# Optimization experiments

Measured on AMD Instinct MI355X. Metric: run time of the kernel, lower is better.

The kernel has to match this reference:

```python
import jax, jax.numpy as jnp
import numpy as np

COMMITMENT_COST = 0.25
EPS = 1e-10


def setup_inputs() -> dict:
    key = jax.random.key(0)
    k0, k1, k2, k3 = jax.random.split(key, 4)
    return {
        "data": jax.random.normal(k0, (16, 4096, 256), dtype=jnp.float32),
        "codebook0": jax.random.normal(k1, (512, 256), dtype=jnp.float32),
        "codebook1": jax.random.normal(k2, (512, 256), dtype=jnp.float32),
        "codebook2": jax.random.normal(k3, (512, 256), dtype=jnp.float32),
        "using": 0,
    }


def _vq_stage(x, cb, beta):
    # x: [N, D] residual; cb: [K, D] codebook
    d = (jnp.sum(x * x, axis=-1, keepdims=True)
         - 2.0 * jnp.einsum('nd,kd->nk', x, cb)
         + jnp.sum(cb * cb, axis=-1))
    idx = jnp.argmin(d, axis=-1)                       # [N]
    enc = jax.nn.one_hot(idx, cb.shape[0], dtype=x.dtype)  # [N, K]
    q = cb[idx]                                        # [N, D] gather
    e_latent = jnp.mean((jax.lax.stop_gradient(q) - x) ** 2)
    q_latent = jnp.mean((q - jax.lax.stop_gradient(x)) ** 2)
    loss = q_latent + beta * e_latent
    q_st = x + jax.lax.stop_gradient(q - x)            # straight-through
    avg_probs = jnp.mean(enc, axis=0)
    entropy = -jnp.sum(avg_probs * jnp.log(avg_probs + EPS))
    return q_st, enc, loss, entropy


def reference(data, codebook0, codebook1, codebook2, using):
    D = data.shape[-1]
    input_shape = data.shape
    flat = data.reshape(-1, D)                         # [N, D]
    codebooks = [codebook0, codebook1, codebook2]
    quantized = jnp.zeros_like(flat)
    total_loss = jnp.float32(0.0)
    total_entropy = jnp.float32(0.0)
    encodings = []
    for stage_cnt, cb in enumerate(codebooks, start=1):
        sub_q, enc, loss, entropy = _vq_stage(flat - quantized, cb, COMMITMENT_COST)
        quantized = quantized + sub_q
        encodings.append(enc)
        total_loss = total_loss + loss
        total_entropy = total_entropy + entropy
        if stage_cnt == using:
            break
    quantized = quantized.reshape(input_shape)
    return (quantized, encodings[0], encodings[1], encodings[2], total_loss, total_entropy)
```

## Files before the change

kernel.cpp:

```cpp
#include <hip/hip_runtime.h>
#include <math.h>

#define NROWS  65536
#define DDIM   256
#define KCODES 512
#define NTH    512
#define NSTAGE 3
#define MARGIN  0.5f
#define MAXFLAG 65536
#define NLOSS   256
#define MB      64
#define RB      8

typedef __attribute__((ext_vector_type(8))) short short8v;
typedef __attribute__((ext_vector_type(4))) float f32x4;

__device__ __forceinline__ unsigned short f2bf(float x) {
  unsigned int u = __float_as_uint(x);
  unsigned int r = (u + 0x7fffu + ((u >> 16) & 1u)) >> 16;
  return (unsigned short)r;
}

__device__ __forceinline__ void glds16(const void* g, void* l) {
  __builtin_amdgcn_global_load_lds(
      (const __attribute__((address_space(1))) unsigned int*)g,
      (__attribute__((address_space(3))) unsigned int*)l, 16, 0, 0);
}

__device__ __forceinline__ float np_sumsq256(const float* p) {
#pragma clang fp contract(off)
  float blk[2];
#pragma unroll
  for (int b = 0; b < 2; ++b) {
    const float* a = p + b * 128;
    float v[16];
#pragma unroll
    for (int l = 0; l < 16; ++l) {
      float p0a = a[l] * a[l];
      float p0b = a[64 + l] * a[64 + l];
      float P0 = p0a + p0b;
      float p1a = a[16 + l] * a[16 + l];
      float p1b = a[80 + l] * a[80 + l];
      float P1 = p1a + p1b;
      float p2a = a[32 + l] * a[32 + l];
      float p2b = a[96 + l] * a[96 + l];
      float P2 = p2a + p2b;
      float p3a = a[48 + l] * a[48 + l];
      float p3b = a[112 + l] * a[112 + l];
      float P3 = p3a + p3b;
      v[l] = (P0 + P1) + (P2 + P3);
    }
    float s1[8];
#pragma unroll
    for (int l = 0; l < 8; ++l) s1[l] = v[l] + v[l + 8];
    float s2[4];
#pragma unroll
    for (int l = 0; l < 4; ++l) s2[l] = s1[l] + s1[l + 4];
    float s3_0 = s2[0] + s2[2];
    float s3_1 = s2[1] + s2[3];
    blk[b] = s3_0 + s3_1;
  }
  return blk[0] + blk[1];
}

__global__ void cc_np_k(const float* __restrict__ c0, const float* __restrict__ c1,
                        const float* __restrict__ c2, float* __restrict__ cc) {
  int t = blockIdx.x * blockDim.x + threadIdx.x;
  if (t >= NSTAGE * KCODES) return;
  const float* cb = (t < KCODES) ? c0 : (t < 2 * KCODES ? c1 : c2);
  cc[t] = np_sumsq256(cb + (size_t)(t & (KCODES - 1)) * DDIM);
}

__global__ void split_cb_k(const float* __restrict__ c0, const float* __restrict__ c1,
                           const float* __restrict__ c2,
                           unsigned short* __restrict__ Ch) {
  int t = blockIdx.x * 256 + threadIdx.x;
  if (t >= NSTAGE * KCODES * 32) return;
  int s = t / (KCODES * 32);
  int rem = t - s * KCODES * 32;
  int code = rem >> 5;
  int gran = rem & 31;
  int chunk = gran >> 2;
  int g = gran & 3;
  int ctile = code >> 6;
  int ct = (code >> 4) & 3;
  int c16 = code & 15;
  const float* cb = (s == 0) ? c0 : (s == 1 ? c1 : c2);
  const float* src = cb + (size_t)code * DDIM + gran * 8;
  unsigned short hv[8];
#pragma unroll
  for (int j = 0; j < 8; ++j) hv[j] = f2bf(src[j]);
  size_t off = (size_t)s * 262144 +
               ((((size_t)(ctile * 8 + chunk) * 4 + ct) * 64) + (g * 16 + c16)) * 16;
  *(uint4*)((char*)Ch + off) = *(uint4*)hv;
}

__global__ __launch_bounds__(256) void chain_k(
    const float* __restrict__ data,
    const float* __restrict__ cbA, const float* __restrict__ cbB,
    const int* __restrict__ idxA, const int* __restrict__ idxB,
    int stage, char* __restrict__ AhG) {
  const int t = blockIdx.x * 256 + threadIdx.x;
  const int r = t >> 5;
  const int g = t & 31;
  const int k0 = g * 8;
  float res[8];
  {
#pragma clang fp contract(off)
    const size_t base = (size_t)r * DDIM + k0;
    int iA = 0, iB = 0;
    if (stage >= 1) iA = idxA[r];
    if (stage == 2) iB = idxB[r];
#pragma unroll
    for (int half = 0; half < 2; ++half) {
      float4 dv = *(const float4*)(data + base + half * 4);
      float x1[4] = {dv.x, dv.y, dv.z, dv.w};
      float rr[4];
      if (stage == 0) {
#pragma unroll
        for (int j = 0; j < 4; ++j) rr[j] = x1[j];
      } else {
        float4 av = *(const float4*)(cbA + (size_t)iA * DDIM + k0 + half * 4);
        float af[4] = {av.x, av.y, av.z, av.w};
        float a[4];
#pragma unroll
        for (int j = 0; j < 4; ++j) a[j] = x1[j] + (af[j] - x1[j]);
        if (stage == 2) {
          float4 bv = *(const float4*)(cbB + (size_t)iB * DDIM + k0 + half * 4);
          float bf[4] = {bv.x, bv.y, bv.z, bv.w};
#pragma unroll
          for (int j = 0; j < 4; ++j) {
            float x2 = x1[j] - a[j];
            float qst2 = x2 + (bf[j] - x2);
            a[j] = a[j] + qst2;
          }
        }
#pragma unroll
        for (int j = 0; j < 4; ++j) rr[j] = x1[j] - a[j];
      }
#pragma unroll
      for (int j = 0; j < 4; ++j) res[half * 4 + j] = rr[j];
    }
  }
  unsigned short hv[8];
#pragma unroll
  for (int j = 0; j < 8; ++j) hv[j] = f2bf(res[j]);
  const int blk = r >> 6, lr = r & 63;
  const size_t byte = (size_t)blk * 32768 + ((lr * 512 + g * 16) ^ ((lr & 7) << 4));
  *(uint4*)(AhG + byte) = *(uint4*)hv;
}

#define A_H_OFF 0
#define RED_OFF 32768
#define SMEM_SZ 40960

__global__ __launch_bounds__(NTH, 1) void gemm_k(
    const char* __restrict__ AhG,
    const unsigned short* __restrict__ Chf,
    const float* __restrict__ ccs,
    int* __restrict__ idx_out, unsigned int* __restrict__ flagcnt,
    int* __restrict__ flagrows) {
  __shared__ char smem[SMEM_SZ];

  const int tid = threadIdx.x;
  const int lane = tid & 63;
  const int w = tid >> 6;
  const int blk = blockIdx.x;
  const int rowbase = blk * MB;

  {
    const char* gh = AhG + (size_t)blk * 32768;
    const int off0 = w * 1024 + lane * 16;
#pragma unroll
    for (int rr2 = 0; rr2 < 4; ++rr2)
      glds16(gh + rr2 * 8192 + off0, smem + A_H_OFF + rr2 * 8192 + off0);
  }

  f32x4 acc[4][4];
#pragma unroll
  for (int rt = 0; rt < 4; ++rt)
#pragma unroll
    for (int ct = 0; ct < 4; ++ct) {
      acc[rt][ct].x = 0.f; acc[rt][ct].y = 0.f;
      acc[rt][ct].z = 0.f; acc[rt][ct].w = 0.f;
    }

  const int g = lane >> 4, c16 = lane & 15;
  const char* bhw = (const char*)Chf + lane * 16;

  __syncthreads();

#pragma clang loop unroll(disable)
  for (int chunk = 0; chunk < 8; ++chunk) {
    short8v ah[4];
#pragma unroll
    for (int rt = 0; rt < 4; ++rt) {
      const int row = rt * 16 + c16;
      const int byte = (row * 512 + (chunk * 4 + g) * 16) ^ ((row & 7) << 4);
      ah[rt] = *(short8v*)(smem + A_H_OFF + byte);
    }
#pragma unroll
    for (int ct = 0; ct < 4; ++ct) {
      short8v bh = *(const short8v*)(bhw + (size_t)((w * 8 + chunk) * 4 + ct) * 1024);
#pragma unroll
      for (int rt = 0; rt < 4; ++rt)
        acc[rt][ct] = __builtin_amdgcn_mfma_f32_16x16x32_bf16(ah[rt], bh, acc[rt][ct], 0, 0, 0);
    }
  }
  __syncthreads();

  float ccv[4];
#pragma unroll
  for (int ct = 0; ct < 4; ++ct) ccv[ct] = ccs[w * 64 + ct * 16 + c16];

  float* red = (float*)(smem + RED_OFF);
#pragma unroll
  for (int rt = 0; rt < 4; ++rt) {
#pragma unroll
    for (int reg = 0; reg < 4; ++reg) {
      const int row = rt * 16 + g * 4 + reg;
      float v1 = 3.0e38f, v2 = 3.0e38f;
      int i1 = 0x7fffffff;
#pragma unroll
      for (int ct = 0; ct < 4; ++ct) {
        const int col = w * 64 + ct * 16 + c16;
        float dd = ccv[ct] - 2.0f * acc[rt][ct][reg];
        if (dd < v1 || (dd == v1 && col < i1)) { v2 = v1; v1 = dd; i1 = col; }
        else if (dd < v2) v2 = dd;
      }
#pragma unroll
      for (int m = 1; m < 16; m <<= 1) {
        float ov1 = __shfl_xor(v1, m, 64);
        int oi1 = __shfl_xor(i1, m, 64);
        float ov2 = __shfl_xor(v2, m, 64);
        float worst = fmaxf(v1, ov1);
        v2 = fminf(fminf(v2, ov2), worst);
        if (ov1 < v1 || (ov1 == v1 && oi1 < i1)) { v1 = ov1; i1 = oi1; }
      }
      if (c16 == 0) {
        float* slot = red + (size_t)(row * 8 + w) * 4;
        slot[0] = v1;
        ((int*)slot)[1] = i1;
        slot[2] = v2;
      }
    }
  }
  __syncthreads();
  if (tid < MB) {
    float v1 = 3.0e38f, v2 = 3.0e38f;
    int i1 = 0x7fffffff;
#pragma unroll
    for (int ww = 0; ww < 8; ++ww) {
      const float* slot = red + (size_t)(tid * 8 + ww) * 4;
      float ov1 = slot[0];
      int oi1 = ((const int*)slot)[1];
      float ov2 = slot[2];
      float worst = fmaxf(v1, ov1);
      v2 = fminf(fminf(v2, ov2), worst);
      if (ov1 < v1 || (ov1 == v1 && oi1 < i1)) { v1 = ov1; i1 = oi1; }
    }
    const int r = rowbase + tid;
    idx_out[r] = i1;
    if (v2 - v1 < MARGIN) {
      unsigned pos = atomicAdd(flagcnt, 1u);
      if (pos < MAXFLAG) flagrows[pos] = r;
    }
  }
}

__global__ __launch_bounds__(256) void refine_k(
    const float* __restrict__ data, const float* __restrict__ cb,
    const float* __restrict__ cbA, const float* __restrict__ cbB,
    const int* __restrict__ idxA, const int* __restrict__ idxB,
    const float* __restrict__ ccs, int stage,
    const unsigned int* __restrict__ flagcnt, const int* __restrict__ flagrows,
    int* __restrict__ idx_out) {
  __shared__ float rows[RB][DDIM];
  __shared__ float xxs[RB];
  __shared__ float red_v[RB][256];
  __shared__ int red_i[RB][256];

  unsigned int n = *flagcnt;
  if (n > MAXFLAG) n = MAXFLAG;
  const int tid = threadIdx.x;

  for (unsigned base = (unsigned)blockIdx.x * RB; base < n;
       base += (unsigned)gridDim.x * RB) {
    const int nb = (int)min((unsigned)RB, n - base);

    for (int u = tid; u < nb * 64; u += 256) {
#pragma clang fp contract(off)
      const int i = u >> 6;
      const int c4 = (u & 63) * 4;
      const int r = flagrows[base + i];
      const size_t gbase = (size_t)r * DDIM + c4;
      float4 dv = *(const float4*)(data + gbase);
      float x1[4] = {dv.x, dv.y, dv.z, dv.w};
      float res[4];
      if (stage == 0) {
#pragma unroll
        for (int j = 0; j < 4; ++j) res[j] = x1[j];
      } else {
        const int iA = idxA[r];
        float4 av = *(const float4*)(cbA + (size_t)iA * DDIM + c4);
        float af[4] = {av.x, av.y, av.z, av.w};
        float a[4];
#pragma unroll
        for (int j = 0; j < 4; ++j) a[j] = x1[j] + (af[j] - x1[j]);
        if (stage == 2) {
          const int iB = idxB[r];
          float4 bv = *(const float4*)(cbB + (size_t)iB * DDIM + c4);
          float bf[4] = {bv.x, bv.y, bv.z, bv.w};
#pragma unroll
          for (int j = 0; j < 4; ++j) {
            float x2 = x1[j] - a[j];
            float qst2 = x2 + (bf[j] - x2);
            a[j] = a[j] + qst2;
          }
        }
#pragma unroll
        for (int j = 0; j < 4; ++j) res[j] = x1[j] - a[j];
      }
#pragma unroll
      for (int j = 0; j < 4; ++j) rows[i][c4 + j] = res[j];
    }
    __syncthreads();
    if (tid < nb) xxs[tid] = np_sumsq256(rows[tid]);
    __syncthreads();

    float bv[RB];
    int bi[RB];
#pragma unroll
    for (int i = 0; i < RB; ++i) { bv[i] = 3.0e38f; bi[i] = 0x7fffffff; }

#pragma clang loop unroll(disable)
    for (int h = 0; h < 2; ++h) {
#pragma clang fp contract(off)
      const int k = tid + h * 256;
      const float* crow = cb + (size_t)k * DDIM;
      float v[RB][4];
#pragma unroll
      for (int i = 0; i < RB; ++i)
#pragma unroll
        for (int l = 0; l < 4; ++l) v[i][l] = 0.f;

#pragma clang loop unroll(disable)
      for (int t = 0; t < 16; ++t) {
        float b[16];
#pragma unroll
        for (int j = 0; j < 16; ++j) b[j] = crow[t * 16 + j];
#pragma unroll
        for (int i = 0; i < RB; ++i) {
#pragma unroll
          for (int l = 0; l < 4; ++l) {
            float a0 = rows[i][t * 16 + l];
            float a1 = rows[i][t * 16 + 4 + l];
            float a2 = rows[i][t * 16 + 8 + l];
            float a3 = rows[i][t * 16 + 12 + l];
            float ab3 = a3 * b[12 + l] + v[i][l];
            float ab2 = a2 * b[8 + l] + ab3;
            float ab1 = a1 * b[4 + l] + ab2;
            v[i][l] = a0 * b[l] + ab1;
          }
        }
      }
      const float cck = ccs[k];
#pragma unroll
      for (int i = 0; i < RB; ++i) {
        float dot = (v[i][0] + v[i][1]) + (v[i][2] + v[i][3]);
        float t1 = xxs[i] - 2.0f * dot;
        float d = t1 + cck;
        if (d < bv[i] || (d == bv[i] && k < bi[i])) { bv[i] = d; bi[i] = k; }
      }
    }

#pragma unroll
    for (int i = 0; i < RB; ++i) { red_v[i][tid] = bv[i]; red_i[i][tid] = bi[i]; }
    __syncthreads();
    for (int gap = 128; gap > 0; gap >>= 1) {
      if (tid < gap) {
#pragma unroll
        for (int i = 0; i < RB; ++i) {
          float o = red_v[i][tid + gap];
          int oi = red_i[i][tid + gap];
          if (o < red_v[i][tid] || (o == red_v[i][tid] && oi < red_i[i][tid])) {
            red_v[i][tid] = o;
            red_i[i][tid] = oi;
          }
        }
      }
      __syncthreads();
    }
    if (tid < nb) idx_out[flagrows[base + tid]] = red_i[tid][0];
    __syncthreads();
  }
}

__global__ __launch_bounds__(256) void final_k(
    const float* __restrict__ data, const float* __restrict__ cb0,
    const float* __restrict__ cb1, const float* __restrict__ cb2,
    const int* __restrict__ idx0, const int* __restrict__ idx1,
    const int* __restrict__ idx2, float* __restrict__ quant,
    float* __restrict__ enc0, float* __restrict__ enc1,
    float* __restrict__ enc2, double* __restrict__ loss_slots,
    unsigned int* __restrict__ hist) {
  __shared__ double wsum[4];
  const int lane = threadIdx.x & 63;
  const int w = threadIdx.x >> 6;
  const int r = blockIdx.x * 4 + w;
  const int i0 = idx0[r], i1 = idx1[r], i2 = idx2[r];
  const size_t base = (size_t)r * DDIM + lane * 4;
  float4 dv = *(const float4*)(data + base);
  float4 c0v = *(const float4*)(cb0 + (size_t)i0 * DDIM + lane * 4);
  float4 c1v = *(const float4*)(cb1 + (size_t)i1 * DDIM + lane * 4);
  float4 c2v = *(const float4*)(cb2 + (size_t)i2 * DDIM + lane * 4);
  float df[4] = {dv.x, dv.y, dv.z, dv.w};
  float q0f[4] = {c0v.x, c0v.y, c0v.z, c0v.w};
  float q1f[4] = {c1v.x, c1v.y, c1v.z, c1v.w};
  float q2f[4] = {c2v.x, c2v.y, c2v.z, c2v.w};
  float qout[4];
  double lsum = 0.0;
  {
#pragma clang fp contract(off)
#pragma unroll
    for (int j = 0; j < 4; ++j) {
      float x1 = df[j];
      float d1 = q0f[j] - x1;
      float qst1 = x1 + d1;
      float a1 = qst1;
      float x2 = x1 - a1;
      float d2 = q1f[j] - x2;
      float qst2 = x2 + d2;
      float a2 = a1 + qst2;
      float x3 = x1 - a2;
      float d3 = q2f[j] - x3;
      float qst3 = x3 + d3;
      float a3 = a2 + qst3;
      qout[j] = a3;
      lsum += (double)d1 * d1 + (double)d2 * d2 + (double)d3 * d3;
    }
  }
  float4 qv = {qout[0], qout[1], qout[2], qout[3]};
  *(float4*)(quant + base) = qv;

#pragma unroll
  for (int off = 1; off < 64; off <<= 1) lsum += __shfl_xor(lsum, off, 64);
  if (lane == 0) {
    wsum[w] = lsum;
    enc0[(size_t)r * KCODES + i0] = 1.0f;
    atomicAdd(&hist[i0], 1u);
  } else if (lane == 1) {
    enc1[(size_t)r * KCODES + i1] = 1.0f;
    atomicAdd(&hist[KCODES + i1], 1u);
  } else if (lane == 2) {
    enc2[(size_t)r * KCODES + i2] = 1.0f;
    atomicAdd(&hist[2 * KCODES + i2], 1u);
  }
  __syncthreads();
  if (threadIdx.x == 0) {
    double bsum = (wsum[0] + wsum[1]) + (wsum[2] + wsum[3]);
    atomicAdd(&loss_slots[blockIdx.x & (NLOSS - 1)], bsum);
  }
}

__global__ void finalize_k(const unsigned int* __restrict__ hist,
                           const double* __restrict__ loss_slots,
                           float* __restrict__ out_scalars) {
  int lane = threadIdx.x;
  double te = 0.0;
  for (int s = 0; s < NSTAGE; ++s) {
    double e = 0.0;
    for (int j = 0; j < KCODES / 64; ++j) {
      int k = j * 64 + lane;
      float pf = (float)hist[s * KCODES + k] * (1.0f / 65536.0f);
      float sf = __fadd_rn(pf, 1e-10f);
      e += (double)pf * log((double)sf);
    }
#pragma unroll
    for (int off = 1; off < 64; off <<= 1) e += __shfl_xor(e, off, 64);
    te += -e;
  }
  double ls = loss_slots[lane] + loss_slots[64 + lane] +
              loss_slots[128 + lane] + loss_slots[192 + lane];
#pragma unroll
  for (int off = 1; off < 64; off <<= 1) ls += __shfl_xor(ls, off, 64);
  if (lane == 0) {
    double tl = 1.25 * ls * (1.0 / 16777216.0);
    out_scalars[0] = (float)tl;
    out_scalars[1] = (float)te;
  }
}

extern "C" void kernel_launch(void* const* d_in, const int* in_sizes, int n_in,
                              void* d_out, int out_size, void* d_ws, size_t ws_size,
                              hipStream_t stream) {
  const float* data = (const float*)d_in[0];
  const float* cb0 = (const float*)d_in[1];
  const float* cb1 = (const float*)d_in[2];
  const float* cb2 = (const float*)d_in[3];
  const float* cbs[3] = {cb0, cb1, cb2};
  float* out = (float*)d_out;
  float* quant = out;
  float* enc0 = out + (size_t)NROWS * DDIM;
  float* enc1 = enc0 + (size_t)NROWS * KCODES;
  float* enc2 = enc1 + (size_t)NROWS * KCODES;
  float* out_scalars = enc2 + (size_t)NROWS * KCODES;

  char* AhG = (char*)enc0;

  double* loss_slots = (double*)d_ws;
  unsigned int* hist = (unsigned int*)((char*)d_ws + 2048);
  unsigned int* flagcnt = (unsigned int*)((char*)d_ws + 8192);
  int* flagrows = (int*)((char*)d_ws + 8320);
  float* cc = (float*)((char*)d_ws + 794752);
  int* idx0 = (int*)((char*)d_ws + 800896);
  int* idx1 = idx0 + NROWS;
  int* idx2 = idx1 + NROWS;
  int* idxs[3] = {idx0, idx1, idx2};
  unsigned short* Ch = (unsigned short*)((char*)d_ws + 1587328);

  hipMemsetAsync(d_ws, 0, 8320, stream);

  cc_np_k<<<(NSTAGE * KCODES + 255) / 256, 256, 0, stream>>>(cb0, cb1, cb2, cc);
  split_cb_k<<<(NSTAGE * KCODES * 32 + 255) / 256, 256, 0, stream>>>(
      cb0, cb1, cb2, Ch);

  for (int s = 0; s < NSTAGE; ++s) {
    chain_k<<<NROWS * 32 / 256, 256, 0, stream>>>(
        data, cb0, cb1, idx0, idx1, s, AhG);
    gemm_k<<<NROWS / MB, NTH, 0, stream>>>(
        AhG,
        (const unsigned short*)((char*)Ch + (size_t)s * 262144),
        cc + s * KCODES, idxs[s], flagcnt + s, flagrows + s * MAXFLAG);
    refine_k<<<512, 256, 0, stream>>>(
        data, cbs[s], cb0, cb1, idx0, idx1, cc + s * KCODES, s,
        flagcnt + s, flagrows + s * MAXFLAG, idxs[s]);
  }

  hipMemsetAsync(enc0, 0, (size_t)3 * NROWS * KCODES * sizeof(float), stream);

  final_k<<<NROWS / 4, 256, 0, stream>>>(
      data, cb0, cb1, cb2, idx0, idx1, idx2, quant, enc0, enc1, enc2,
      loss_slots, hist);

  finalize_k<<<1, 64, 0, stream>>>(hist, loss_slots, out_scalars);
}
```

Before: 537.3 us.

## Use split-bf16 three-product GEMM and tighten refine margin

Splits the residuals and codebooks into high and low bf16 parts and accumulates hi*hi + hi*lo + lo*hi with MFMA, so the distance GEMM is close to fp32 accuracy. The near-tie margin that flags rows for exact fp32 refinement drops from 0.5 to 0.025, which should sharply cut the number of rows refine_k has to recompute. The cost is triple the MFMA work, twice the LDS and A-tile traffic, and an extra low-part codebook buffer in the workspace.

```diff
diff --git a/kernel.cpp b/kernel.cpp
--- a/kernel.cpp
+++ b/kernel.cpp
@@ -6,7 +6,7 @@
 #define KCODES 512
 #define NTH    512
 #define NSTAGE 3
-#define MARGIN  0.5f
+#define MARGIN  2.5e-2f
 #define MAXFLAG 65536
 #define NLOSS   256
 #define MB      64
@@ -19,6 +19,9 @@
   unsigned int u = __float_as_uint(x);
   unsigned int r = (u + 0x7fffu + ((u >> 16) & 1u)) >> 16;
   return (unsigned short)r;
+}
+__device__ __forceinline__ float bf2f(unsigned short h) {
+  return __uint_as_float(((unsigned int)h) << 16);
 }
 
 __device__ __forceinline__ void glds16(const void* g, void* l) {
@@ -73,7 +76,8 @@
 
 __global__ void split_cb_k(const float* __restrict__ c0, const float* __restrict__ c1,
                            const float* __restrict__ c2,
-                           unsigned short* __restrict__ Ch) {
+                           unsigned short* __restrict__ Ch,
+                           unsigned short* __restrict__ Cl) {
   int t = blockIdx.x * 256 + threadIdx.x;
   if (t >= NSTAGE * KCODES * 32) return;
   int s = t / (KCODES * 32);
@@ -87,19 +91,25 @@
   int c16 = code & 15;
   const float* cb = (s == 0) ? c0 : (s == 1 ? c1 : c2);
   const float* src = cb + (size_t)code * DDIM + gran * 8;
-  unsigned short hv[8];
-#pragma unroll
-  for (int j = 0; j < 8; ++j) hv[j] = f2bf(src[j]);
+  unsigned short hv[8], lv[8];
+#pragma unroll
+  for (int j = 0; j < 8; ++j) {
+    float x = src[j];
+    unsigned short h = f2bf(x);
+    hv[j] = h;
+    lv[j] = f2bf(x - bf2f(h));
+  }
   size_t off = (size_t)s * 262144 +
                ((((size_t)(ctile * 8 + chunk) * 4 + ct) * 64) + (g * 16 + c16)) * 16;
   *(uint4*)((char*)Ch + off) = *(uint4*)hv;
+  *(uint4*)((char*)Cl + off) = *(uint4*)lv;
 }
 
 __global__ __launch_bounds__(256) void chain_k(
     const float* __restrict__ data,
     const float* __restrict__ cbA, const float* __restrict__ cbB,
     const int* __restrict__ idxA, const int* __restrict__ idxB,
-    int stage, char* __restrict__ AhG) {
+    int stage, char* __restrict__ AhG, char* __restrict__ AlG) {
   const int t = blockIdx.x * 256 + threadIdx.x;
   const int r = t >> 5;
   const int g = t & 31;
@@ -142,21 +152,27 @@
       for (int j = 0; j < 4; ++j) res[half * 4 + j] = rr[j];
     }
   }
-  unsigned short hv[8];
-#pragma unroll
-  for (int j = 0; j < 8; ++j) hv[j] = f2bf(res[j]);
+  unsigned short hv[8], lv[8];
+#pragma unroll
+  for (int j = 0; j < 8; ++j) {
+    unsigned short h = f2bf(res[j]);
+    hv[j] = h;
+    lv[j] = f2bf(res[j] - bf2f(h));
+  }
   const int blk = r >> 6, lr = r & 63;
   const size_t byte = (size_t)blk * 32768 + ((lr * 512 + g * 16) ^ ((lr & 7) << 4));
   *(uint4*)(AhG + byte) = *(uint4*)hv;
+  *(uint4*)(AlG + byte) = *(uint4*)lv;
 }
 
 #define A_H_OFF 0
-#define RED_OFF 32768
-#define SMEM_SZ 40960
+#define A_L_OFF 32768
+#define RED_OFF 65536
+#define SMEM_SZ 73728
 
 __global__ __launch_bounds__(NTH, 1) void gemm_k(
-    const char* __restrict__ AhG,
-    const unsigned short* __restrict__ Chf,
+    const char* __restrict__ AhG, const char* __restrict__ AlG,
+    const unsigned short* __restrict__ Chf, const unsigned short* __restrict__ Clf,
     const float* __restrict__ ccs,
     int* __restrict__ idx_out, unsigned int* __restrict__ flagcnt,
     int* __restrict__ flagrows) {
@@ -170,10 +186,13 @@
 
   {
     const char* gh = AhG + (size_t)blk * 32768;
+    const char* gl = AlG + (size_t)blk * 32768;
     const int off0 = w * 1024 + lane * 16;
 #pragma unroll
-    for (int rr2 = 0; rr2 < 4; ++rr2)
+    for (int rr2 = 0; rr2 < 4; ++rr2) {
       glds16(gh + rr2 * 8192 + off0, smem + A_H_OFF + rr2 * 8192 + off0);
+      glds16(gl + rr2 * 8192 + off0, smem + A_L_OFF + rr2 * 8192 + off0);
+    }
   }
 
   f32x4 acc[4][4];
@@ -187,24 +206,30 @@
 
   const int g = lane >> 4, c16 = lane & 15;
   const char* bhw = (const char*)Chf + lane * 16;
+  const char* blw = (const char*)Clf + lane * 16;
 
   __syncthreads();
 
 #pragma clang loop unroll(disable)
   for (int chunk = 0; chunk < 8; ++chunk) {
-    short8v ah[4];
+    short8v ah[4], al[4];
 #pragma unroll
     for (int rt = 0; rt < 4; ++rt) {
       const int row = rt * 16 + c16;
       const int byte = (row * 512 + (chunk * 4 + g) * 16) ^ ((row & 7) << 4);
       ah[rt] = *(short8v*)(smem + A_H_OFF + byte);
+      al[rt] = *(short8v*)(smem + A_L_OFF + byte);
     }
 #pragma unroll
     for (int ct = 0; ct < 4; ++ct) {
       short8v bh = *(const short8v*)(bhw + (size_t)((w * 8 + chunk) * 4 + ct) * 1024);
-#pragma unroll
-      for (int rt = 0; rt < 4; ++rt)
+      short8v bl = *(const short8v*)(blw + (size_t)((w * 8 + chunk) * 4 + ct) * 1024);
+#pragma unroll
+      for (int rt = 0; rt < 4; ++rt) {
         acc[rt][ct] = __builtin_amdgcn_mfma_f32_16x16x32_bf16(ah[rt], bh, acc[rt][ct], 0, 0, 0);
+        acc[rt][ct] = __builtin_amdgcn_mfma_f32_16x16x32_bf16(ah[rt], bl, acc[rt][ct], 0, 0, 0);
+        acc[rt][ct] = __builtin_amdgcn_mfma_f32_16x16x32_bf16(al[rt], bh, acc[rt][ct], 0, 0, 0);
+      }
     }
   }
   __syncthreads();
@@ -507,6 +532,7 @@
   float* out_scalars = enc2 + (size_t)NROWS * KCODES;
 
   char* AhG = (char*)enc0;
+  char* AlG = AhG + (size_t)NROWS * 512;
 
   double* loss_slots = (double*)d_ws;
   unsigned int* hist = (unsigned int*)((char*)d_ws + 2048);
@@ -518,19 +544,21 @@
   int* idx2 = idx1 + NROWS;
   int* idxs[3] = {idx0, idx1, idx2};
   unsigned short* Ch = (unsigned short*)((char*)d_ws + 1587328);
+  unsigned short* Cl = (unsigned short*)((char*)d_ws + 2373760);
 
   hipMemsetAsync(d_ws, 0, 8320, stream);
 
   cc_np_k<<<(NSTAGE * KCODES + 255) / 256, 256, 0, stream>>>(cb0, cb1, cb2, cc);
   split_cb_k<<<(NSTAGE * KCODES * 32 + 255) / 256, 256, 0, stream>>>(
-      cb0, cb1, cb2, Ch);
+      cb0, cb1, cb2, Ch, Cl);
 
   for (int s = 0; s < NSTAGE; ++s) {
     chain_k<<<NROWS * 32 / 256, 256, 0, stream>>>(
-        data, cb0, cb1, idx0, idx1, s, AhG);
+        data, cb0, cb1, idx0, idx1, s, AhG, AlG);
     gemm_k<<<NROWS / MB, NTH, 0, stream>>>(
-        AhG,
+        AhG, AlG,
         (const unsigned short*)((char*)Ch + (size_t)s * 262144),
+        (const unsigned short*)((char*)Cl + (size_t)s * 262144),
         cc + s * KCODES, idxs[s], flagcnt + s, flagrows + s * MAXFLAG);
     refine_k<<<512, 256, 0, stream>>>(
         data, cbs[s], cb0, cb1, idx0, idx1, cc + s * KCODES, s,
```

New measurement: 567.5 us. 5.6% more time.
